# Optimization experiments

Hardware: AMD Instinct MI355X
Metric: run time of the kernel (lower is better)

## Reference

```python
import jax, jax.numpy as jnp
import numpy as np

KH = KW = 3  # kernel spatial size is hard-coded to 3 in the original layer


def _tdiv2(x):
    # matches tf.cast(x / 2, tf.int32): true-divide by 2, truncate toward zero
    return jnp.trunc(x * 0.5)


def setup_inputs() -> dict:
    key = jax.random.key(0)
    k1, k2, k3 = jax.random.split(key, 3)
    B, H, W, C, F = 4, 32, 32, 64, 128
    # integer-valued tensors stored as float32 (bit-serial math needs integer weights)
    inputs = jax.random.randint(k1, (B, H, W, C), 0, 16).astype(jnp.float32)
    kernel = jax.random.randint(k2, (KH, KW, C, F), -8, 8).astype(jnp.float32)
    bias = jax.random.randint(k3, (F,), -4, 4).astype(jnp.float32)
    return {"inputs": inputs, "kernel": kernel, "bias": bias, "bits": 4}


def reference(inputs, kernel, bias, bits):
    # Bit-serial conv2d, padding='same' (pad=1), activation='relu'.
    # Per (kernel position, input element, output channel) the original computes
    #   acc <- trunc((acc + x * (w mod 2) * sign(w_orig)) / 2); w <- trunc(w / 2)
    # for `bits` iterations, then sums over channels/kernel window.
    B, H, W, C = inputs.shape
    F = kernel.shape[-1]
    x = jnp.pad(inputs, ((0, 0), (1, 1), (1, 1), (0, 0)))  # 'same' padding, pad=1
    out = jnp.zeros((B, H, W, F), inputs.dtype)
    for i in range(KH):
        for j in range(KW):
            patch = x[:, i:i + H, j:j + W, :][..., None]   # [B,H,W,C,1]
            w = kernel[i, j]                               # [C,F]
            s = jnp.sign(w)                                # sign of ORIGINAL weight, fixed
            acc = jnp.zeros((B, H, W, C, F), inputs.dtype)
            ww = w
            for _ in range(bits):
                acc = _tdiv2(acc + patch * (jnp.mod(ww, 2.0) * s))
                ww = _tdiv2(ww)
            out = out + acc.sum(axis=3)                    # sum over C; kernel window summed by loop
    return jax.nn.relu(out + bias)
```

## Files before the change

### kernel.cpp

```cpp
#include <hip/hip_runtime.h>
#include <stdint.h>


typedef short s16x2 __attribute__((ext_vector_type(2)));

#define NWPK 36864
#define XOFF 36864
#define NXPK 147968

__global__ __launch_bounds__(256) void prep_all(const float* __restrict__ kern,
                                                const float* __restrict__ input,
                                                uint32_t* __restrict__ ws) {
    int bid = blockIdx.x, tid = threadIdx.x;
    if (bid < 144) {
        int t  = bid * 256 + tid;
        int e  = t & 3;
        int f  = (t >> 2) & 127;
        int c8 = (t >> 9) & 7;
        int ki = t >> 12;
        int c  = c8 * 8 + e * 2;
        int wlo = (int)kern[(ki * 64 + c    ) * 128 + f];
        int whi = (int)kern[(ki * 64 + c + 1) * 128 + f];
        ws[t] = (uint32_t)(uint16_t)(int16_t)wlo |
                ((uint32_t)(uint16_t)(int16_t)whi << 16);
    } else {
        int t = (bid - 144) * 256 + tid;
        if (t >= NXPK) return;
        int c2    = t & 31;
        int rest  = t >> 5;
        int wp    = rest % 34;
        int rest2 = rest / 34;
        int hp    = rest2 % 34;
        int b     = rest2 / 34;
        int v = 0;
        if (hp >= 1 && hp <= 32 && wp >= 1 && wp <= 32) {
            const float* p = &input[(((b * 32) + hp - 1) * 32 + (wp - 1)) * 64 + c2 * 2];
            v = (int)p[0] | ((int)p[1] << 16);
        }
        ws[XOFF + t] = (uint32_t)v;
    }
}

__global__ __launch_bounds__(128, 4) void conv_main(const uint32_t* __restrict__ ws,
                                                    const float* __restrict__ bias,
                                                    float* __restrict__ out) {
    const uint32_t* wpk = ws;
    const uint32_t* xpk = ws + XOFF;

    int bid   = blockIdx.x;
    int wpair = bid & 15;
    int h     = (bid >> 4) & 31;
    int b     = bid >> 9;
    int f     = threadIdx.x;
    int w0    = wpair * 2;

    __shared__ uint32_t patch[3 * 4 * 32];

    #pragma unroll
    for (int k = 0; k < 3; ++k) {
        int idx  = k * 128 + f;
        int c2   = idx & 31;
        int colr = idx >> 5;
        int col  = colr & 3;
        int r    = colr >> 2;
        patch[idx] = xpk[((b * 34 + h + r) * 34 + (w0 + col)) * 32 + c2];
    }
    __syncthreads();

    s16x2 acc0 = {0, 0}, acc1 = {0, 0};

    for (int i = 0; i < 3; ++i) {
        for (int j = 0; j < 3; ++j) {
            int ki = i * 3 + j;
            const uint32_t* wrow = wpk + (ki * 1024 + f) * 4;
            const uint32_t* px   = patch + (i * 4 + j) * 32;
            #pragma unroll
            for (int c8 = 0; c8 < 8; ++c8) {
                int4 wv = *(const int4*)(wrow + c8 * 512);
                int4 x0 = *(const int4*)(px + c8 * 4);
                int4 x1 = *(const int4*)(px + 32 + c8 * 4);
                #pragma unroll
                for (int e = 0; e < 4; ++e) {
                    s16x2 w2 = __builtin_bit_cast(s16x2, (&wv.x)[e]);
                    s16x2 A  = (w2 >> 15) & (short)15;
                    s16x2 t0 = (__builtin_bit_cast(s16x2, (&x0.x)[e]) * w2 + A) >> 4;
                    s16x2 t1 = (__builtin_bit_cast(s16x2, (&x1.x)[e]) * w2 + A) >> 4;
                    acc0 += t0;
                    acc1 += t1;
                }
            }
        }
    }

    int bi   = (int)bias[f];
    int base = ((b * 32 + h) * 32 + w0) * 128 + f;
    int a;
    a = __builtin_bit_cast(int, acc0);
    { int r0 = (int)(short)(a & 0xffff) + (a >> 16) + bi;
      out[base]       = (float)(r0 < 0 ? 0 : r0); }
    a = __builtin_bit_cast(int, acc1);
    { int r1 = (int)(short)(a & 0xffff) + (a >> 16) + bi;
      out[base + 128] = (float)(r1 < 0 ? 0 : r1); }
}

extern "C" void kernel_launch(void* const* d_in, const int* in_sizes, int n_in,
                              void* d_out, int out_size, void* d_ws, size_t ws_size,
                              hipStream_t stream) {
    const float* input  = (const float*)d_in[0];
    const float* kernel = (const float*)d_in[1];
    const float* bias   = (const float*)d_in[2];

    uint32_t* ws = (uint32_t*)d_ws;

    prep_all<<<144 + 579, 256, 0, stream>>>(kernel, input, ws);
    conv_main<<<2048, 128, 0, stream>>>(ws, bias, (float*)d_out);
}
```

Before: 80.97 us.

## Split channels across threads, hold weights in registers, 8 pixels per block

The conv kernel now runs 512-thread blocks, each covering 8 output pixels. Each thread handles one filter and a quarter of the channels, with its 18 int4 weight vectors preloaded into registers. The weight packing layout changes to match. Partial sums from the four channel groups are reduced through shared memory before bias and ReLU. The aim is to reuse each loaded weight across 8 pixels instead of 2, cutting global weight traffic, at the cost of higher register pressure, an extra barrier and the reduction step.

```diff
diff --git a/kernel.cpp b/kernel.cpp
--- a/kernel.cpp
+++ b/kernel.cpp
@@ -14,11 +14,13 @@
     int bid = blockIdx.x, tid = threadIdx.x;
     if (bid < 144) {
         int t  = bid * 256 + tid;
-        int e  = t & 3;
+        int u  = t & 3;
         int f  = (t >> 2) & 127;
-        int c8 = (t >> 9) & 7;
-        int ki = t >> 12;
-        int c  = c8 * 8 + e * 2;
+        int cq = (t >> 9) & 3;
+        int gk = t >> 11;
+        int g  = gk & 1;
+        int ki = gk >> 1;
+        int c  = cq * 16 + g * 8 + u * 2;
         int wlo = (int)kern[(ki * 64 + c    ) * 128 + f];
         int whi = (int)kern[(ki * 64 + c + 1) * 128 + f];
         ws[t] = (uint32_t)(uint16_t)(int16_t)wlo |
@@ -41,66 +43,81 @@
     }
 }
 
-__global__ __launch_bounds__(128, 4) void conv_main(const uint32_t* __restrict__ ws,
+__global__ __launch_bounds__(512, 4) void conv_main(const uint32_t* __restrict__ ws,
                                                     const float* __restrict__ bias,
                                                     float* __restrict__ out) {
-    const uint32_t* wpk = ws;
     const uint32_t* xpk = ws + XOFF;
 
-    int bid   = blockIdx.x;
-    int wpair = bid & 15;
-    int h     = (bid >> 4) & 31;
-    int b     = bid >> 9;
-    int f     = threadIdx.x;
-    int w0    = wpair * 2;
+    int bid = blockIdx.x;
+    int wt  = bid & 3;
+    int h   = (bid >> 2) & 31;
+    int b   = bid >> 7;
+    int tid = threadIdx.x;
+    int f   = tid & 127;
+    int cq  = tid >> 7;
+    int w0  = wt * 8;
 
-    __shared__ uint32_t patch[3 * 4 * 32];
+    __shared__ uint32_t xl[3 * 10 * 32];
+    __shared__ int prt[4 * 8 * 128];
+
+    for (int k = tid; k < 960; k += 512) {
+        int c2  = k & 31;
+        int rc  = k >> 5;
+        int col = rc % 10;
+        int r   = rc / 10;
+        xl[k] = xpk[((b * 34 + h + r) * 34 + (w0 + col)) * 32 + c2];
+    }
+
+    int4 wv[18];
+    const int4* wp = (const int4*)ws;
+    #pragma unroll
+    for (int i = 0; i < 18; ++i) wv[i] = wp[i * 512 + tid];
+
+    __syncthreads();
+
+    s16x2 acc[8] = {};
 
     #pragma unroll
-    for (int k = 0; k < 3; ++k) {
-        int idx  = k * 128 + f;
-        int c2   = idx & 31;
-        int colr = idx >> 5;
-        int col  = colr & 3;
-        int r    = colr >> 2;
-        patch[idx] = xpk[((b * 34 + h + r) * 34 + (w0 + col)) * 32 + c2];
-    }
-    __syncthreads();
-
-    s16x2 acc0 = {0, 0}, acc1 = {0, 0};
-
-    for (int i = 0; i < 3; ++i) {
-        for (int j = 0; j < 3; ++j) {
-            int ki = i * 3 + j;
-            const uint32_t* wrow = wpk + (ki * 1024 + f) * 4;
-            const uint32_t* px   = patch + (i * 4 + j) * 32;
+    for (int ki = 0; ki < 9; ++ki) {
+        const int row = ki / 3, jj = ki % 3;
+        #pragma unroll
+        for (int g = 0; g < 2; ++g) {
+            const int4 w4 = wv[ki * 2 + g];
+            const uint32_t* xrow = xl + (row * 10 + jj) * 32 + cq * 8 + g * 4;
             #pragma unroll
-            for (int c8 = 0; c8 < 8; ++c8) {
-                int4 wv = *(const int4*)(wrow + c8 * 512);
-                int4 x0 = *(const int4*)(px + c8 * 4);
-                int4 x1 = *(const int4*)(px + 32 + c8 * 4);
+            for (int pb = 0; pb < 2; ++pb) {
+                int4 xv0 = *(const int4*)(xrow + (pb * 4 + 0) * 32);
+                int4 xv1 = *(const int4*)(xrow + (pb * 4 + 1) * 32);
+                int4 xv2 = *(const int4*)(xrow + (pb * 4 + 2) * 32);
+                int4 xv3 = *(const int4*)(xrow + (pb * 4 + 3) * 32);
                 #pragma unroll
-                for (int e = 0; e < 4; ++e) {
-                    s16x2 w2 = __builtin_bit_cast(s16x2, (&wv.x)[e]);
+                for (int u = 0; u < 4; ++u) {
+                    s16x2 w2 = __builtin_bit_cast(s16x2, (&w4.x)[u]);
                     s16x2 A  = (w2 >> 15) & (short)15;
-                    s16x2 t0 = (__builtin_bit_cast(s16x2, (&x0.x)[e]) * w2 + A) >> 4;
-                    s16x2 t1 = (__builtin_bit_cast(s16x2, (&x1.x)[e]) * w2 + A) >> 4;
-                    acc0 += t0;
-                    acc1 += t1;
+                    acc[pb*4+0] += (__builtin_bit_cast(s16x2, (&xv0.x)[u]) * w2 + A) >> 4;
+                    acc[pb*4+1] += (__builtin_bit_cast(s16x2, (&xv1.x)[u]) * w2 + A) >> 4;
+                    acc[pb*4+2] += (__builtin_bit_cast(s16x2, (&xv2.x)[u]) * w2 + A) >> 4;
+                    acc[pb*4+3] += (__builtin_bit_cast(s16x2, (&xv3.x)[u]) * w2 + A) >> 4;
                 }
             }
         }
     }
 
-    int bi   = (int)bias[f];
-    int base = ((b * 32 + h) * 32 + w0) * 128 + f;
-    int a;
-    a = __builtin_bit_cast(int, acc0);
-    { int r0 = (int)(short)(a & 0xffff) + (a >> 16) + bi;
-      out[base]       = (float)(r0 < 0 ? 0 : r0); }
-    a = __builtin_bit_cast(int, acc1);
-    { int r1 = (int)(short)(a & 0xffff) + (a >> 16) + bi;
-      out[base + 128] = (float)(r1 < 0 ? 0 : r1); }
+    #pragma unroll
+    for (int px = 0; px < 8; ++px) {
+        int a = __builtin_bit_cast(int, acc[px]);
+        prt[(cq * 8 + px) * 128 + f] = (int)(short)(a & 0xffff) + (a >> 16);
+    }
+    __syncthreads();
+
+    for (int k = tid; k < 1024; k += 512) {
+        int ff = k & 127;
+        int px = k >> 7;
+        int v = prt[px * 128 + ff] + prt[(8 + px) * 128 + ff] +
+                prt[(16 + px) * 128 + ff] + prt[(24 + px) * 128 + ff] +
+                (int)bias[ff];
+        out[((b * 32 + h) * 32 + w0 + px) * 128 + ff] = (float)(v < 0 ? 0 : v);
+    }
 }
 
 extern "C" void kernel_launch(void* const* d_in, const int* in_sizes, int n_in,
@@ -113,5 +130,5 @@
     uint32_t* ws = (uint32_t*)d_ws;
 
     prep_all<<<144 + 579, 256, 0, stream>>>(kernel, input, ws);
-    conv_main<<<2048, 128, 0, stream>>>(ws, bias, (float*)d_out);
+    conv_main<<<512, 512, 0, stream>>>(ws, bias, (float*)d_out);
 }
```

After: 81.47 us. About the same (+0.6%).
